# Kernel tuning notes

Measured on AMD Instinct MI355X. Metric: run time of the kernel, lower is better.

Reference implementation:

```python
import jax, jax.numpy as jnp
import numpy as np

H = 16
D_MODEL = 1024
D_K = D_MODEL // H
MAX_REL = 16
REL_VOCAB = 2 * MAX_REL + 1


def _rel_pos_ids(seq_len):
    r = jnp.arange(seq_len)
    dist = r[None, :] - r[:, None]                      # [S,S]
    return jnp.clip(dist, -MAX_REL, MAX_REL) + MAX_REL  # in [0, 2*MAX_REL]


def setup_inputs() -> dict:
    key = jax.random.key(0)
    ks = jax.random.split(key, 16)
    B, S = 2, 2048
    f32 = jnp.float32
    inp = {
        "query": jax.random.normal(ks[0], (B, S, D_MODEL), f32),
        "key": jax.random.normal(ks[1], (B, S, D_MODEL), f32),
        "value": jax.random.normal(ks[2], (B, S, D_MODEL), f32),
        # four nn.Linear(d_model, d_model): W [out,in], b [out]
        "Wq": jax.random.normal(ks[3], (D_MODEL, D_MODEL), f32) * 0.02,
        "bq": jnp.zeros((D_MODEL,), f32),
        "Wk": jax.random.normal(ks[4], (D_MODEL, D_MODEL), f32) * 0.02,
        "bk": jnp.zeros((D_MODEL,), f32),
        "Wv": jax.random.normal(ks[5], (D_MODEL, D_MODEL), f32) * 0.02,
        "bv": jnp.zeros((D_MODEL,), f32),
        "Wo": jax.random.normal(ks[6], (D_MODEL, D_MODEL), f32) * 0.02,
        "bo": jnp.zeros((D_MODEL,), f32),
        # relative-position embedding tables (keys and values)
        "rel_k_table": jax.random.normal(ks[7], (REL_VOCAB, D_K), f32) * 0.02,
        "rel_v_table": jax.random.normal(ks[8], (REL_VOCAB, D_K), f32) * 0.02,
    }
    return inp


def reference(query, key, value, Wq, bq, Wk, bk, Wv, bv, Wo, bo,
              rel_k_table, rel_v_table):
    B, S, E = query.shape
    ids = _rel_pos_ids(S)                    # [S,S] int
    rel_k = rel_k_table[ids]                 # [S,S,d_k]
    rel_v = rel_v_table[ids]                 # [S,S,d_k]

    def proj(x, W, b):
        y = x @ W.T + b                      # [B,S,E]
        return y.reshape(B, S, H, D_K).transpose(0, 2, 1, 3)  # [B,H,S,d_k]

    q = proj(query, Wq, bq)
    k = proj(key, Wk, bk)
    v = proj(value, Wv, bv)

    # NOTE: original has no 1/sqrt(d_k) scaling and ignores mask — faithful.
    logits = jnp.einsum('bhqd,bhkd->bhqk', q, k) \
           + jnp.einsum('bhqd,qkd->bhqk', q, rel_k)
    w = jax.nn.softmax(logits, axis=-1)      # [B,H,S,S]

    x = jnp.einsum('bhqk,bhkd->bhqd', w, v) \
      + jnp.einsum('bhqk,qkd->bhqd', w, rel_v)

    x = x.transpose(0, 2, 1, 3).reshape(B, S, H * D_K)
    return x @ Wo.T + bo
```

## Files before the change

### kernel.cpp

```cpp
#include <hip/hip_runtime.h>
#include <hip/hip_bf16.h>

typedef unsigned short u16;
typedef __attribute__((ext_vector_type(8))) short short8;
typedef __attribute__((ext_vector_type(4))) short short4_t;
typedef __attribute__((ext_vector_type(4))) float f32x4;

#define MFMA16(a, b, c) __builtin_amdgcn_mfma_f32_16x16x32_bf16((a), (b), (c), 0, 0, 0)

#if __has_builtin(__builtin_amdgcn_mfma_f32_16x16x16bf16_1k)
#define MFMAK16(a, b, c) __builtin_amdgcn_mfma_f32_16x16x16bf16_1k((a), (b), (c), 0, 0, 0)
#elif __has_builtin(__builtin_amdgcn_mfma_f32_16x16x16_bf16)
#define MFMAK16(a, b, c) __builtin_amdgcn_mfma_f32_16x16x16_bf16((a), (b), (c), 0, 0, 0)
#else
__device__ __forceinline__ f32x4 mfmak16_asm(short4_t a, short4_t b, f32x4 c) {
  asm("v_mfma_f32_16x16x16_bf16 %0, %1, %2, %0" : "+v"(c) : "v"(a), "v"(b));
  return c;
}
#define MFMAK16(a, b, c) mfmak16_asm((a), (b), (c))
#endif

#define GLOAD_LDS16(gp, lp)                                          \
  __builtin_amdgcn_global_load_lds(                                  \
      (const __attribute__((address_space(1))) void*)(gp),           \
      (__attribute__((address_space(3))) void*)(lp), 16, 0, 0)
#define SBAR() asm volatile("s_barrier" ::: "memory")
#define WAIT_LGKM0() asm volatile("s_waitcnt lgkmcnt(0)" ::: "memory")
#define WAIT_VM0() asm volatile("s_waitcnt vmcnt(0)" ::: "memory")

#define LOG2E 1.44269504088896340736f

__device__ __forceinline__ float us2f(u16 u) {
  union { unsigned int i; float f; } c; c.i = ((unsigned int)u) << 16; return c.f;
}
__device__ __forceinline__ u16 f2us(float f) {
  union { float f; unsigned int i; } c; c.f = f;
  return (u16)((c.i + 0x7fffu + ((c.i >> 16) & 1u)) >> 16);
}
__device__ __forceinline__ unsigned int f2us2(float a, float b) {
  union { __hip_bfloat162 h; unsigned int u; } c;
  c.h = __float22bfloat162_rn(float2{a, b});
  return c.u;
}
__device__ __forceinline__ float exp2fast(float x) {
#if __has_builtin(__builtin_amdgcn_exp2f)
  return __builtin_amdgcn_exp2f(x);
#else
  return exp2f(x);
#endif
}

__global__ __launch_bounds__(256) void cvt_all_kernel(
    const float* x0, const float* x1, const float* x2, const float* w0,
    const float* w1, const float* w2, const float* w3, const float* relk,
    u16* y0, u16* y1, u16* y2, u16* z0, u16* z1, u16* z2, u16* z3,
    u16* relkb) {
  const int z = blockIdx.z;
  if (z == 7) {
    const int i = (blockIdx.x * 256 + threadIdx.x) * 8;
    if (i < 4096) {
      if (i < 2112) {
        const float4 a = *(const float4*)(relk + i);
        const float4 b = *(const float4*)(relk + i + 4);
        unsigned int o[4];
        o[0] = f2us2(a.x, a.y); o[1] = f2us2(a.z, a.w);
        o[2] = f2us2(b.x, b.y); o[3] = f2us2(b.z, b.w);
        *(uint4*)(relkb + i) = *(uint4*)o;
      } else {
        uint4 zz = {0u, 0u, 0u, 0u};
        *(uint4*)(relkb + i) = zz;
      }
    }
    return;
  }
  const float* src; u16* dst; int n;
  switch (z) {
    case 0: src = x0; dst = y0; n = 4194304; break;
    case 1: src = x1; dst = y1; n = 4194304; break;
    case 2: src = x2; dst = y2; n = 4194304; break;
    case 3: src = w0; dst = z0; n = 1048576; break;
    case 4: src = w1; dst = z1; n = 1048576; break;
    case 5: src = w2; dst = z2; n = 1048576; break;
    default: src = w3; dst = z3; n = 1048576; break;
  }
  const int i = (blockIdx.x * 256 + threadIdx.x) * 8;
  if (i < n) {
    const float4 a = *(const float4*)(src + i);
    const float4 b = *(const float4*)(src + i + 4);
    unsigned int o[4];
    o[0] = f2us2(a.x, a.y); o[1] = f2us2(a.z, a.w);
    o[2] = f2us2(b.x, b.y); o[3] = f2us2(b.z, b.w);
    *(uint4*)(dst + i) = *(uint4*)o;
  }
}

template <int MODE, typename OUT>
__device__ __forceinline__ void gemm_body(u16* __restrict__ SM,
                                          const u16* __restrict__ X,
                                          const u16* __restrict__ W,
                                          const float* __restrict__ bias,
                                          OUT* __restrict__ Y, int row0, int col0,
                                          float oscale) {
  u16* As = SM;
  u16* Bs = SM + 8192;
  const int tid = threadIdx.x;
  const int lane = tid & 63;
  const int wid = tid >> 6;
  const int wm = wid >> 1, wn = wid & 1;
  const int l15 = lane & 15, l16 = lane >> 4;
  const int lrow = lane >> 3;
  const int lchunk = (lane & 7) ^ lrow;

  f32x4 acc[4][4];
#pragma unroll
  for (int i = 0; i < 4; i++)
#pragma unroll
    for (int j = 0; j < 4; j++) acc[i][j] = (f32x4){0.f, 0.f, 0.f, 0.f};

  for (int k0 = 0; k0 < 1024; k0 += 64) {
#pragma unroll
    for (int i = 0; i < 4; i++) {
      const int rb = wid * 32 + i * 8;
      GLOAD_LDS16(X + (size_t)(row0 + rb + lrow) * 1024 + k0 + lchunk * 8, &As[rb * 64]);
      GLOAD_LDS16(W + (size_t)(col0 + rb + lrow) * 1024 + k0 + lchunk * 8, &Bs[rb * 64]);
    }
    __syncthreads();
#pragma unroll
    for (int kk = 0; kk < 2; kk++) {
      const int ch = kk * 4 + l16;
      short8 af[4], bfr[4];
#pragma unroll
      for (int t = 0; t < 4; t++) {
        const int m = wm * 64 + t * 16 + l15;
        af[t] = *(const short8*)&As[m * 64 + ((ch ^ (m & 7)) * 8)];
        const int n = wn * 64 + t * 16 + l15;
        bfr[t] = *(const short8*)&Bs[n * 64 + ((ch ^ (n & 7)) * 8)];
      }
#pragma unroll
      for (int tm = 0; tm < 4; tm++)
#pragma unroll
        for (int tn = 0; tn < 4; tn++)
          acc[tm][tn] = MFMA16(af[tm], bfr[tn], acc[tm][tn]);
    }
    __syncthreads();
  }

  if (MODE == 0) {
#pragma unroll
    for (int tn = 0; tn < 4; tn++) {
      const int col = col0 + wn * 64 + tn * 16 + l15;
      const float bv = bias[col];
#pragma unroll
      for (int tm = 0; tm < 4; tm++) {
        const int rowb = row0 + wm * 64 + tm * 16 + l16 * 4;
#pragma unroll
        for (int r = 0; r < 4; r++)
          Y[(size_t)(rowb + r) * 1024 + col] = (OUT)(acc[tm][tn][r] + bv);
      }
    }
  } else {
    u16* T = SM;
    const int bb = row0 >> 11;
    const int sbase = row0 & 2047;
#pragma unroll
    for (int pass = 0; pass < 2; pass++) {
      __syncthreads();
      if (wm == pass) {
#pragma unroll
        for (int tn = 0; tn < 4; tn++) {
          const int coll = wn * 64 + tn * 16 + l15;
          const float bv = bias[col0 + coll];
#pragma unroll
          for (int tm = 0; tm < 4; tm++) {
            if (MODE == 1) {
#pragma unroll
              for (int r = 0; r < 4; r++)
                T[(tm * 16 + l16 * 4 + r) * 136 + coll] = f2us((acc[tm][tn][r] + bv) * oscale);
            } else {
              unsigned int o[2];
              o[0] = f2us2(acc[tm][tn][0] + bv, acc[tm][tn][1] + bv);
              o[1] = f2us2(acc[tm][tn][2] + bv, acc[tm][tn][3] + bv);
              *(short4_t*)&T[coll * 72 + tm * 16 + l16 * 4] = *(short4_t*)o;
            }
          }
        }
      }
      __syncthreads();
      if (MODE == 1) {
#pragma unroll
        for (int i = 0; i < 8; i++) {
          const int idx = tid + i * 256;
          const int srow = idx >> 5, c4 = idx & 31;
          const short4_t v = *(const short4_t*)&T[srow * 136 + c4 * 4];
          const int col = col0 + c4 * 4;
          const int hh = col >> 6, dd = col & 63;
          const int s = sbase + pass * 64 + srow;
          *(short4_t*)&((u16*)Y)[(((size_t)(bb * 16 + hh)) * 2048 + s) * 64 + dd] = v;
        }
      } else {
#pragma unroll
        for (int i = 0; i < 4; i++) {
          const int idx = tid + i * 256;
          const int cl = idx >> 3, sc = idx & 7;
          const short8 v = *(const short8*)&T[cl * 72 + sc * 8];
          const int col = col0 + cl;
          const int hh = col >> 6, dd = col & 63;
          const int s = sbase + pass * 64 + sc * 8;
          *(short8*)&((u16*)Y)[(((size_t)(bb * 16 + hh)) * 64 + dd) * 2048 + s] = v;
        }
      }
    }
  }
}

__global__ __launch_bounds__(256) void qkv_kernel(
    const u16* Xq, const u16* Xk, const u16* Xv, const u16* Wq, const u16* Wk,
    const u16* Wv, const float* bq, const float* bk, const float* bv, u16* Yq,
    u16* Yk, u16* Yv) {
  __shared__ __align__(16) u16 SM[16384];
  const int z = blockIdx.z;
  const u16* X = z == 0 ? Xq : (z == 1 ? Xk : Xv);
  const u16* W = z == 0 ? Wq : (z == 1 ? Wk : Wv);
  const float* bi = z == 0 ? bq : (z == 1 ? bk : bv);
  u16* Y = z == 0 ? Yq : (z == 1 ? Yk : Yv);
  if (z == 2)
    gemm_body<2, u16>(SM, X, W, bi, Y, blockIdx.x * 128, blockIdx.y * 128, 1.0f);
  else
    gemm_body<1, u16>(SM, X, W, bi, Y, blockIdx.x * 128, blockIdx.y * 128,
                      z == 0 ? LOG2E : 1.0f);
}

__global__ __launch_bounds__(256) void oproj_kernel(const u16* Xc, const u16* Wo,
                                                    const float* bo, float* out) {
  __shared__ __align__(16) u16 SM[16384];
  gemm_body<0, float>(SM, Xc, Wo, bo, out, blockIdx.x * 128, blockIdx.y * 128, 1.0f);
}

__global__ __launch_bounds__(256, 6) void attn_kernel(
    const u16* __restrict__ Qg, const u16* __restrict__ Kg,
    const u16* __restrict__ Vtg, const u16* __restrict__ relkb,
    const float* __restrict__ relv, u16* __restrict__ ctx) {
  __shared__ __align__(16) u16 KV[8192];
  __shared__ __align__(16) u16 qrelJ[64 * 33];
  __shared__ __align__(16) u16 wsum[64 * 31];

  const int tid = threadIdx.x, lane = tid & 63, wid = tid >> 6;
  const int l15 = lane & 15, l16 = lane >> 4;
  const int bh = blockIdx.x;
  const int b = bh >> 4, h = bh & 15;
  const int by = blockIdx.y;
  const int q0 = by * 64;
  const u16* Qb = Qg + (size_t)bh * 2048 * 64;
  const u16* Kb = Kg + (size_t)bh * 2048 * 64;
  const u16* Vtb = Vtg + (size_t)bh * 64 * 2048;

  const int lrow = lane >> 3;
  const int lchunk = (lane & 7) ^ lrow;
  const int qw = wid * 16;
  const int kq4 = l16 * 4;
  const int qrow = qw + l15;

#pragma unroll
  for (int i = 0; i < 2; i++) {
    const int rb = qw + i * 8;
    GLOAD_LDS16(Qb + (size_t)(q0 + rb + lrow) * 64 + lchunk * 8, &KV[rb * 64]);
  }
  for (int idx = tid; idx < 992; idx += 256) ((unsigned int*)wsum)[idx] = 0u;
  __syncthreads();

  short8 aq[2];
  {
    const int m = qw + l15;
    aq[0] = *(const short8*)&KV[m * 64 + ((l16 ^ (m & 7)) * 8)];
    aq[1] = *(const short8*)&KV[m * 64 + (((4 + l16) ^ (m & 7)) * 8)];
  }
  {
    f32x4 qa[3];
#pragma unroll
    for (int nt = 0; nt < 3; nt++) {
      qa[nt] = (f32x4){0.f, 0.f, 0.f, 0.f};
#pragma unroll
      for (int kk = 0; kk < 2; kk++) {
        const short8 bf =
            *(const short8*)(relkb + (nt * 16 + l15) * 64 + kk * 32 + l16 * 8);
        qa[nt] = MFMA16(aq[kk], bf, qa[nt]);
      }
    }
#pragma unroll
    for (int nt = 0; nt < 3; nt++) {
      if (nt < 2 || l15 == 0) {
#pragma unroll
        for (int r = 0; r < 4; r++)
          qrelJ[(qw + kq4 + r) * 33 + nt * 16 + l15] = f2us(qa[nt][r]);
      }
    }
  }
  WAIT_LGKM0();
  const float q0r = us2f(qrelJ[qrow * 33 + 0]);
  const float q32r = us2f(qrelJ[qrow * 33 + 32]);
  const f32x4 ebl = (f32x4){q0r, q0r, q0r, q0r};
  const f32x4 ebr = (f32x4){q32r, q32r, q32r, q32r};
  const f32x4 zf = (f32x4){0.f, 0.f, 0.f, 0.f};
  const short4_t ones4 = (short4_t){(short)0x3F80, (short)0x3F80,
                                    (short)0x3F80, (short)0x3F80};

  float wl_p = 0.f, wr_p = 0.f;
  f32x4 SL = zf, SR = zf, SD = zf;
  f32x4 Oacc[4];
#pragma unroll
  for (int t = 0; t < 4; t++) Oacc[t] = zf;

  auto stage = [&](int k0c) {
    SBAR();
#pragma unroll
    for (int i = 0; i < 2; i++) {
      const int rb = qw + i * 8;
      GLOAD_LDS16(Kb + (size_t)(k0c + rb + lrow) * 64 + lchunk * 8, &KV[rb * 64]);
    }
#pragma unroll
    for (int i = 0; i < 2; i++) {
      const int rb = qw + i * 8;
      GLOAD_LDS16(Vtb + (size_t)(rb + lrow) * 2048 + k0c + lchunk * 8,
                  &KV[4096 + rb * 64]);
    }
    WAIT_VM0();
    SBAR();
  };

  auto qk = [&](int tn, f32x4 cin) -> f32x4 {
    const int n = tn * 16 + l15;
    const short8 bk0 = *(const short8*)&KV[n * 64 + ((l16 ^ (n & 7)) * 8)];
    const short8 bk1 = *(const short8*)&KV[n * 64 + (((4 + l16) ^ (n & 7)) * 8)];
    f32x4 s = MFMA16(bk0, aq[0], cin);
    s = MFMA16(bk1, aq[1], s);
    return s;
  };

  auto pvstep = [&](const short4_t* pf) {
    __builtin_amdgcn_s_setprio(1);
#pragma unroll
    for (int td = 0; td < 4; td++) {
      const int row = td * 16 + l15;
      const int rs = row & 7;
#pragma unroll
      for (int kk = 0; kk < 4; kk++) {
        const short4_t vf = *(const short4_t*)&KV[4096 + row * 64 +
                                                  (((kk * 2 + (l16 >> 1)) ^ rs) * 8) +
                                                  (l16 & 1) * 4];
        Oacc[td] = MFMAK16(vf, pf[kk], Oacc[td]);
      }
    }
    __builtin_amdgcn_s_setprio(0);
  };

  auto psum = [&](const short4_t* pf, f32x4& S) {
#pragma unroll
    for (int kk = 0; kk < 4; kk++) S = MFMAK16(ones4, pf[kk], S);
  };

  auto offdiag = [&](f32x4 ebv, f32x4& S) {
    short4_t pf[4];
#pragma unroll
    for (int tn = 0; tn < 4; tn++) {
      const f32x4 sac = qk(tn, ebv);
      union { unsigned int u[2]; short4_t s; } c;
      c.u[0] = f2us2(exp2fast(sac[0]), exp2fast(sac[1]));
      c.u[1] = f2us2(exp2fast(sac[2]), exp2fast(sac[3]));
      pf[tn] = c.s;
    }
    pvstep(pf);
    psum(pf, S);
  };

  auto diag = [&](int k0) {
    short4_t pf[4];
#pragma unroll
    for (int tn = 0; tn < 4; tn++) {
      const f32x4 sac = qk(tn, zf);
      float pv4[4];
#pragma unroll
      for (int r = 0; r < 4; r++) {
        const int kg = k0 + tn * 16 + kq4 + r;
        const int dlt = kg - (q0 + qrow);
        const int jj = (dlt < -16 ? -16 : (dlt > 16 ? 16 : dlt)) + 16;
        const float p = exp2fast(sac[r] + us2f(qrelJ[qrow * 33 + jj]));
        pv4[r] = p;
        if (dlt <= -16) wl_p += p;
        else if (dlt >= 16) wr_p += p;
        else wsum[qrow * 31 + (dlt + 15)] = f2us(p);
      }
      union { unsigned int u[2]; short4_t s; } c;
      c.u[0] = f2us2(pv4[0], pv4[1]);
      c.u[1] = f2us2(pv4[2], pv4[3]);
      pf[tn] = c.s;
    }
    pvstep(pf);
    psum(pf, SD);
  };

  const int dlo = (by >= 1) ? by - 1 : 0;
  const int dhi = (by + 2 <= 32) ? by + 2 : 32;
  for (int kt = 0; kt < dlo; ++kt) { stage(kt * 64); offdiag(ebl, SL); }
  for (int kt = dlo; kt < dhi; ++kt) { stage(kt * 64); diag(kt * 64); }
  for (int kt = dhi; kt < 32; ++kt) { stage(kt * 64); offdiag(ebr, SR); }

  wl_p += __shfl_xor(wl_p, 16); wl_p += __shfl_xor(wl_p, 32);
  wr_p += __shfl_xor(wr_p, 16); wr_p += __shfl_xor(wr_p, 32);
  const float l_total = SL[0] + SR[0] + SD[0];
  const float linv = 1.f / l_total;
  const float wl = (SL[0] + wl_p) * linv;
  const float wr = (SR[0] + wr_p) * linv;

#pragma unroll
  for (int td = 0; td < 4; td++) {
    const f32x4 rv0 = *(const f32x4*)&relv[td * 16 + kq4];
    const f32x4 rv32 = *(const f32x4*)&relv[32 * 64 + td * 16 + kq4];
#pragma unroll
    for (int r = 0; r < 4; r++)
      Oacc[td][r] = Oacc[td][r] * linv + wl * rv0[r] + wr * rv32[r];
  }
  WAIT_LGKM0();
  for (int j = 1; j <= 31; j++) {
    const float wv = us2f(wsum[qrow * 31 + (j - 1)]) * linv;
#pragma unroll
    for (int td = 0; td < 4; td++) {
      const f32x4 rv = *(const f32x4*)&relv[j * 64 + td * 16 + kq4];
#pragma unroll
      for (int r = 0; r < 4; r++) Oacc[td][r] += wv * rv[r];
    }
  }
  SBAR();
#pragma unroll
  for (int td = 0; td < 4; td++) {
    unsigned int o[2];
    o[0] = f2us2(Oacc[td][0], Oacc[td][1]);
    o[1] = f2us2(Oacc[td][2], Oacc[td][3]);
    *(short4_t*)&KV[qrow * 72 + td * 16 + kq4] = *(short4_t*)o;
  }
  WAIT_LGKM0();
  SBAR();
#pragma unroll
  for (int i = 0; i < 2; i++) {
    const int idx = tid + i * 256;
    const int q = idx >> 3, sc = idx & 7;
    const short8 v = *(const short8*)&KV[q * 72 + sc * 8];
    *(short8*)&ctx[((size_t)b * 2048 + q0 + q) * 1024 + h * 64 + sc * 8] = v;
  }
}

extern "C" void kernel_launch(void* const* d_in, const int* in_sizes, int n_in,
                              void* d_out, int out_size, void* d_ws, size_t ws_size,
                              hipStream_t stream) {
  u16* qb = (u16*)d_ws;
  u16* kb = qb + 4194304;
  u16* vtb = kb + 4194304;
  u16* ctx = vtb + 4194304;
  u16* Xq = ctx + 4194304;
  u16* Xk = Xq + 4194304;
  u16* Xv = Xk + 4194304;
  u16* Wqb = Xv + 4194304;
  u16* Wkb = Wqb + 1048576;
  u16* Wvb = Wkb + 1048576;
  u16* Wob = Wvb + 1048576;
  u16* relkb = Wob + 1048576;

  const float* bq = (const float*)d_in[4];
  const float* bk = (const float*)d_in[6];
  const float* bv = (const float*)d_in[8];
  const float* bo = (const float*)d_in[10];
  const float* relk = (const float*)d_in[11];
  const float* relv = (const float*)d_in[12];

  dim3 blk(256);
  cvt_all_kernel<<<dim3(2048, 1, 8), blk, 0, stream>>>(
      (const float*)d_in[0], (const float*)d_in[1], (const float*)d_in[2],
      (const float*)d_in[3], (const float*)d_in[5], (const float*)d_in[7],
      (const float*)d_in[9], relk, Xq, Xk, Xv, Wqb, Wkb, Wvb, Wob, relkb);
  qkv_kernel<<<dim3(32, 8, 3), blk, 0, stream>>>(Xq, Xk, Xv, Wqb, Wkb, Wvb, bq,
                                                 bk, bv, qb, kb, vtb);
  attn_kernel<<<dim3(32, 32), blk, 0, stream>>>(qb, kb, vtb, relkb, relv, ctx);
  oproj_kernel<<<dim3(32, 8), blk, 0, stream>>>(ctx, Wob, bo, (float*)d_out);
}
```

Before: 263.2 us.

## Load V fragments directly to registers, MFMA rel-V epilogue, smaller o-proj tiles

The attention kernel now loads V^T fragments straight from global memory into registers one tile ahead, instead of staging them through LDS, and stages only K in shared memory. The scalar 31-step rel_v accumulation loop is replaced by bf16 MFMAs over the wsum fragments, with wsum padded to 32 columns. The output projection GEMM is templated to use 64x64 tiles with a 4x larger grid, and the attention launch bound occupancy hint drops from 6 to 4. This trades LDS traffic and scalar FMA work for more VGPR pressure and slightly lower rel_v precision.

Result: slower. 422.6 us (+60.6%).

```diff
diff --git a/kernel.cpp b/kernel.cpp
--- a/kernel.cpp
+++ b/kernel.cpp
@@ -94,15 +94,16 @@
   }
 }
 
-template <int MODE, typename OUT>
+template <int MODE, typename OUT, int BM, int BN>
 __device__ __forceinline__ void gemm_body(u16* __restrict__ SM,
                                           const u16* __restrict__ X,
                                           const u16* __restrict__ W,
                                           const float* __restrict__ bias,
                                           OUT* __restrict__ Y, int row0, int col0,
                                           float oscale) {
+  constexpr int TM = BM / 32, TN = BN / 32;
   u16* As = SM;
-  u16* Bs = SM + 8192;
+  u16* Bs = SM + BM * 64;
   const int tid = threadIdx.x;
   const int lane = tid & 63;
   const int wid = tid >> 6;
@@ -111,35 +112,42 @@
   const int lrow = lane >> 3;
   const int lchunk = (lane & 7) ^ lrow;
 
-  f32x4 acc[4][4];
-#pragma unroll
-  for (int i = 0; i < 4; i++)
-#pragma unroll
-    for (int j = 0; j < 4; j++) acc[i][j] = (f32x4){0.f, 0.f, 0.f, 0.f};
+  f32x4 acc[TM][TN];
+#pragma unroll
+  for (int i = 0; i < TM; i++)
+#pragma unroll
+    for (int j = 0; j < TN; j++) acc[i][j] = (f32x4){0.f, 0.f, 0.f, 0.f};
 
   for (int k0 = 0; k0 < 1024; k0 += 64) {
 #pragma unroll
-    for (int i = 0; i < 4; i++) {
-      const int rb = wid * 32 + i * 8;
+    for (int i = 0; i < TM; i++) {
+      const int rb = (wid * TM + i) * 8;
       GLOAD_LDS16(X + (size_t)(row0 + rb + lrow) * 1024 + k0 + lchunk * 8, &As[rb * 64]);
+    }
+#pragma unroll
+    for (int i = 0; i < TN; i++) {
+      const int rb = (wid * TN + i) * 8;
       GLOAD_LDS16(W + (size_t)(col0 + rb + lrow) * 1024 + k0 + lchunk * 8, &Bs[rb * 64]);
     }
     __syncthreads();
 #pragma unroll
     for (int kk = 0; kk < 2; kk++) {
       const int ch = kk * 4 + l16;
-      short8 af[4], bfr[4];
-#pragma unroll
-      for (int t = 0; t < 4; t++) {
-        const int m = wm * 64 + t * 16 + l15;
+      short8 af[TM], bfr[TN];
+#pragma unroll
+      for (int t = 0; t < TM; t++) {
+        const int m = wm * (BM / 2) + t * 16 + l15;
         af[t] = *(const short8*)&As[m * 64 + ((ch ^ (m & 7)) * 8)];
-        const int n = wn * 64 + t * 16 + l15;
+      }
+#pragma unroll
+      for (int t = 0; t < TN; t++) {
+        const int n = wn * (BN / 2) + t * 16 + l15;
         bfr[t] = *(const short8*)&Bs[n * 64 + ((ch ^ (n & 7)) * 8)];
       }
 #pragma unroll
-      for (int tm = 0; tm < 4; tm++)
-#pragma unroll
-        for (int tn = 0; tn < 4; tn++)
+      for (int tm = 0; tm < TM; tm++)
+#pragma unroll
+        for (int tn = 0; tn < TN; tn++)
           acc[tm][tn] = MFMA16(af[tm], bfr[tn], acc[tm][tn]);
     }
     __syncthreads();
@@ -147,12 +155,12 @@
 
   if (MODE == 0) {
 #pragma unroll
-    for (int tn = 0; tn < 4; tn++) {
-      const int col = col0 + wn * 64 + tn * 16 + l15;
+    for (int tn = 0; tn < TN; tn++) {
+      const int col = col0 + wn * (BN / 2) + tn * 16 + l15;
       const float bv = bias[col];
 #pragma unroll
-      for (int tm = 0; tm < 4; tm++) {
-        const int rowb = row0 + wm * 64 + tm * 16 + l16 * 4;
+      for (int tm = 0; tm < TM; tm++) {
+        const int rowb = row0 + wm * (BM / 2) + tm * 16 + l16 * 4;
 #pragma unroll
         for (int r = 0; r < 4; r++)
           Y[(size_t)(rowb + r) * 1024 + col] = (OUT)(acc[tm][tn][r] + bv);
@@ -167,11 +175,11 @@
       __syncthreads();
       if (wm == pass) {
 #pragma unroll
-        for (int tn = 0; tn < 4; tn++) {
+        for (int tn = 0; tn < TN; tn++) {
           const int coll = wn * 64 + tn * 16 + l15;
           const float bv = bias[col0 + coll];
 #pragma unroll
-          for (int tm = 0; tm < 4; tm++) {
+          for (int tm = 0; tm < TM; tm++) {
             if (MODE == 1) {
 #pragma unroll
               for (int r = 0; r < 4; r++)
@@ -224,25 +232,25 @@
   const float* bi = z == 0 ? bq : (z == 1 ? bk : bv);
   u16* Y = z == 0 ? Yq : (z == 1 ? Yk : Yv);
   if (z == 2)
-    gemm_body<2, u16>(SM, X, W, bi, Y, blockIdx.x * 128, blockIdx.y * 128, 1.0f);
+    gemm_body<2, u16, 128, 128>(SM, X, W, bi, Y, blockIdx.x * 128, blockIdx.y * 128, 1.0f);
   else
-    gemm_body<1, u16>(SM, X, W, bi, Y, blockIdx.x * 128, blockIdx.y * 128,
-                      z == 0 ? LOG2E : 1.0f);
+    gemm_body<1, u16, 128, 128>(SM, X, W, bi, Y, blockIdx.x * 128, blockIdx.y * 128,
+                                z == 0 ? LOG2E : 1.0f);
 }
 
 __global__ __launch_bounds__(256) void oproj_kernel(const u16* Xc, const u16* Wo,
                                                     const float* bo, float* out) {
-  __shared__ __align__(16) u16 SM[16384];
-  gemm_body<0, float>(SM, Xc, Wo, bo, out, blockIdx.x * 128, blockIdx.y * 128, 1.0f);
-}
-
-__global__ __launch_bounds__(256, 6) void attn_kernel(
+  __shared__ __align__(16) u16 SM[8192];
+  gemm_body<0, float, 64, 64>(SM, Xc, Wo, bo, out, blockIdx.x * 64, blockIdx.y * 64, 1.0f);
+}
+
+__global__ __launch_bounds__(256, 4) void attn_kernel(
     const u16* __restrict__ Qg, const u16* __restrict__ Kg,
     const u16* __restrict__ Vtg, const u16* __restrict__ relkb,
     const float* __restrict__ relv, u16* __restrict__ ctx) {
-  __shared__ __align__(16) u16 KV[8192];
+  __shared__ __align__(16) u16 KO[4608];
   __shared__ __align__(16) u16 qrelJ[64 * 33];
-  __shared__ __align__(16) u16 wsum[64 * 31];
+  __shared__ __align__(16) u16 wsum[64 * 32];
 
   const int tid = threadIdx.x, lane = tid & 63, wid = tid >> 6;
   const int l15 = lane & 15, l16 = lane >> 4;
@@ -260,19 +268,33 @@
   const int kq4 = l16 * 4;
   const int qrow = qw + l15;
 
+  unsigned int voff[4];
+#pragma unroll
+  for (int td = 0; td < 4; td++) voff[td] = (unsigned)((td * 16 + l15) * 2048 + l16 * 4);
+  short4_t vf[4][4];
+  auto issueV = [&](int k0c) {
+#pragma unroll
+    for (int td = 0; td < 4; td++)
+#pragma unroll
+      for (int kk = 0; kk < 4; kk++)
+        vf[td][kk] = *(const short4_t*)(Vtb + voff[td] + k0c + kk * 16);
+  };
+
+  issueV(0);
+
 #pragma unroll
   for (int i = 0; i < 2; i++) {
     const int rb = qw + i * 8;
-    GLOAD_LDS16(Qb + (size_t)(q0 + rb + lrow) * 64 + lchunk * 8, &KV[rb * 64]);
-  }
-  for (int idx = tid; idx < 992; idx += 256) ((unsigned int*)wsum)[idx] = 0u;
+    GLOAD_LDS16(Qb + (size_t)(q0 + rb + lrow) * 64 + lchunk * 8, &KO[rb * 64]);
+  }
+  for (int idx = tid; idx < 1024; idx += 256) ((unsigned int*)wsum)[idx] = 0u;
   __syncthreads();
 
   short8 aq[2];
   {
     const int m = qw + l15;
-    aq[0] = *(const short8*)&KV[m * 64 + ((l16 ^ (m & 7)) * 8)];
-    aq[1] = *(const short8*)&KV[m * 64 + (((4 + l16) ^ (m & 7)) * 8)];
+    aq[0] = *(const short8*)&KO[m * 64 + ((l16 ^ (m & 7)) * 8)];
+    aq[1] = *(const short8*)&KO[m * 64 + (((4 + l16) ^ (m & 7)) * 8)];
   }
   {
     f32x4 qa[3];
@@ -310,27 +332,10 @@
 #pragma unroll
   for (int t = 0; t < 4; t++) Oacc[t] = zf;
 
-  auto stage = [&](int k0c) {
-    SBAR();
-#pragma unroll
-    for (int i = 0; i < 2; i++) {
-      const int rb = qw + i * 8;
-      GLOAD_LDS16(Kb + (size_t)(k0c + rb + lrow) * 64 + lchunk * 8, &KV[rb * 64]);
-    }
-#pragma unroll
-    for (int i = 0; i < 2; i++) {
-      const int rb = qw + i * 8;
-      GLOAD_LDS16(Vtb + (size_t)(rb + lrow) * 2048 + k0c + lchunk * 8,
-                  &KV[4096 + rb * 64]);
-    }
-    WAIT_VM0();
-    SBAR();
-  };
-
   auto qk = [&](int tn, f32x4 cin) -> f32x4 {
     const int n = tn * 16 + l15;
-    const short8 bk0 = *(const short8*)&KV[n * 64 + ((l16 ^ (n & 7)) * 8)];
-    const short8 bk1 = *(const short8*)&KV[n * 64 + (((4 + l16) ^ (n & 7)) * 8)];
+    const short8 bk0 = *(const short8*)&KO[n * 64 + ((l16 ^ (n & 7)) * 8)];
+    const short8 bk1 = *(const short8*)&KO[n * 64 + (((4 + l16) ^ (n & 7)) * 8)];
     f32x4 s = MFMA16(bk0, aq[0], cin);
     s = MFMA16(bk1, aq[1], s);
     return s;
@@ -339,17 +344,10 @@
   auto pvstep = [&](const short4_t* pf) {
     __builtin_amdgcn_s_setprio(1);
 #pragma unroll
-    for (int td = 0; td < 4; td++) {
-      const int row = td * 16 + l15;
-      const int rs = row & 7;
-#pragma unroll
-      for (int kk = 0; kk < 4; kk++) {
-        const short4_t vf = *(const short4_t*)&KV[4096 + row * 64 +
-                                                  (((kk * 2 + (l16 >> 1)) ^ rs) * 8) +
-                                                  (l16 & 1) * 4];
-        Oacc[td] = MFMAK16(vf, pf[kk], Oacc[td]);
-      }
-    }
+    for (int td = 0; td < 4; td++)
+#pragma unroll
+      for (int kk = 0; kk < 4; kk++)
+        Oacc[td] = MFMAK16(vf[td][kk], pf[kk], Oacc[td]);
     __builtin_amdgcn_s_setprio(0);
   };
 
@@ -387,7 +385,7 @@
         pv4[r] = p;
         if (dlt <= -16) wl_p += p;
         else if (dlt >= 16) wr_p += p;
-        else wsum[qrow * 31 + (dlt + 15)] = f2us(p);
+        else wsum[qrow * 32 + (dlt + 15)] = f2us(p);
       }
       union { unsigned int u[2]; short4_t s; } c;
       c.u[0] = f2us2(pv4[0], pv4[1]);
@@ -400,9 +398,21 @@
 
   const int dlo = (by >= 1) ? by - 1 : 0;
   const int dhi = (by + 2 <= 32) ? by + 2 : 32;
-  for (int kt = 0; kt < dlo; ++kt) { stage(kt * 64); offdiag(ebl, SL); }
-  for (int kt = dlo; kt < dhi; ++kt) { stage(kt * 64); diag(kt * 64); }
-  for (int kt = dhi; kt < 32; ++kt) { stage(kt * 64); offdiag(ebr, SR); }
+  for (int kt = 0; kt < 32; ++kt) {
+    const int k0 = kt * 64;
+    SBAR();
+#pragma unroll
+    for (int i = 0; i < 2; i++) {
+      const int rb = qw + i * 8;
+      GLOAD_LDS16(Kb + (size_t)(k0 + rb + lrow) * 64 + lchunk * 8, &KO[rb * 64]);
+    }
+    WAIT_VM0();
+    SBAR();
+    if (kt < dlo)       offdiag(ebl, SL);
+    else if (kt >= dhi) offdiag(ebr, SR);
+    else                diag(k0);
+    if (kt < 31) issueV(k0 + 64);
+  }
 
   wl_p += __shfl_xor(wl_p, 16); wl_p += __shfl_xor(wl_p, 32);
   wr_p += __shfl_xor(wr_p, 16); wr_p += __shfl_xor(wr_p, 32);
@@ -411,6 +421,30 @@
   const float wl = (SL[0] + wl_p) * linv;
   const float wr = (SR[0] + wr_p) * linv;
 
+  {
+    short4_t relf[4][2];
+#pragma unroll
+    for (int td = 0; td < 4; td++)
+#pragma unroll
+      for (int kk = 0; kk < 2; kk++) {
+        const int jb = kk * 16 + l16 * 4 + 1;
+        const int d = td * 16 + l15;
+        union { unsigned int u[2]; short4_t s; } c;
+        c.u[0] = f2us2(relv[(jb + 0) * 64 + d], relv[(jb + 1) * 64 + d]);
+        c.u[1] = f2us2(relv[(jb + 2) * 64 + d], relv[(jb + 3) * 64 + d]);
+        relf[td][kk] = c.s;
+      }
+    short4_t wfrag[2];
+#pragma unroll
+    for (int kk = 0; kk < 2; kk++)
+      wfrag[kk] = *(const short4_t*)&wsum[qrow * 32 + kk * 16 + l16 * 4];
+#pragma unroll
+    for (int td = 0; td < 4; td++)
+#pragma unroll
+      for (int kk = 0; kk < 2; kk++)
+        Oacc[td] = MFMAK16(relf[td][kk], wfrag[kk], Oacc[td]);
+  }
+
 #pragma unroll
   for (int td = 0; td < 4; td++) {
     const f32x4 rv0 = *(const f32x4*)&relv[td * 16 + kq4];
@@ -419,23 +453,14 @@
     for (int r = 0; r < 4; r++)
       Oacc[td][r] = Oacc[td][r] * linv + wl * rv0[r] + wr * rv32[r];
   }
-  WAIT_LGKM0();
-  for (int j = 1; j <= 31; j++) {
-    const float wv = us2f(wsum[qrow * 31 + (j - 1)]) * linv;
-#pragma unroll
-    for (int td = 0; td < 4; td++) {
-      const f32x4 rv = *(const f32x4*)&relv[j * 64 + td * 16 + kq4];
-#pragma unroll
-      for (int r = 0; r < 4; r++) Oacc[td][r] += wv * rv[r];
-    }
-  }
+
   SBAR();
 #pragma unroll
   for (int td = 0; td < 4; td++) {
     unsigned int o[2];
     o[0] = f2us2(Oacc[td][0], Oacc[td][1]);
     o[1] = f2us2(Oacc[td][2], Oacc[td][3]);
-    *(short4_t*)&KV[qrow * 72 + td * 16 + kq4] = *(short4_t*)o;
+    *(short4_t*)&KO[qrow * 72 + td * 16 + kq4] = *(short4_t*)o;
   }
   WAIT_LGKM0();
   SBAR();
@@ -443,7 +468,7 @@
   for (int i = 0; i < 2; i++) {
     const int idx = tid + i * 256;
     const int q = idx >> 3, sc = idx & 7;
-    const short8 v = *(const short8*)&KV[q * 72 + sc * 8];
+    const short8 v = *(const short8*)&KO[q * 72 + sc * 8];
     *(short8*)&ctx[((size_t)b * 2048 + q0 + q) * 1024 + h * 64 + sc * 8] = v;
   }
 }
@@ -479,5 +504,5 @@
   qkv_kernel<<<dim3(32, 8, 3), blk, 0, stream>>>(Xq, Xk, Xv, Wqb, Wkb, Wvb, bq,
                                                  bk, bv, qb, kb, vtb);
   attn_kernel<<<dim3(32, 32), blk, 0, stream>>>(qb, kb, vtb, relkb, relv, ctx);
-  oproj_kernel<<<dim3(32, 8), blk, 0, stream>>>(ctx, Wob, bo, (float*)d_out);
-}
+  oproj_kernel<<<dim3(64, 16), blk, 0, stream>>>(ctx, Wob, bo, (float*)d_out);
+}
```
